# Optimization experiments

Measured on AMD Instinct MI355X. Metric: run time of the kernel, lower is better.

## Reference

```python
import jax, jax.numpy as jnp
import numpy as np
import math

B, S, D = 4, 2048, 768
H, DH = 12, 64  # num heads, head dim; H*DH == D


def setup_inputs() -> dict:
    key = jax.random.key(0)
    ks = jax.random.split(key, 10)
    q = jax.random.normal(ks[0], (B, S, D), jnp.float32)
    k = jax.random.normal(ks[1], (B, S, D), jnp.float32)
    v = jax.random.normal(ks[2], (B, S, D), jnp.float32)
    attention_mask = jax.random.bernoulli(ks[3], 0.1, (B, S, S))
    s = 1.0 / math.sqrt(D)
    # Linear weights stored as [in, out] so projection is x @ W + b
    Wq = jax.random.uniform(ks[4], (D, D), jnp.float32, -s, s)
    bq = jax.random.uniform(ks[5], (D,), jnp.float32, -s, s)
    Wk = jax.random.uniform(ks[6], (D, D), jnp.float32, -s, s)
    bk = jax.random.uniform(ks[7], (D,), jnp.float32, -s, s)
    Wv = jax.random.uniform(ks[8], (D, D), jnp.float32, -s, s)
    bv = jax.random.uniform(ks[9], (D,), jnp.float32, -s, s)
    return {"q": q, "k": k, "v": v, "attention_mask": attention_mask,
            "Wq": Wq, "bq": bq, "Wk": Wk, "bk": bk, "Wv": Wv, "bv": bv}


def _split_heads(x):
    # [B, S, D] -> [B, H, S, DH]
    return x.reshape(B, -1, H, DH).transpose(0, 2, 1, 3)


def reference(q, k, v, attention_mask, Wq, bq, Wk, bk, Wv, bv):
    Q = _split_heads(q @ Wq + bq)
    K = _split_heads(k @ Wk + bk)
    V = _split_heads(v @ Wv + bv)
    scores = jnp.einsum('bhqd,bhkd->bhqk', Q, K) / math.sqrt(DH)
    # masked_fill(mask, -1e9); 3-dim mask broadcasts over heads
    scores = jnp.where(attention_mask[:, None, :, :], -1.0e9, scores)
    probs = jax.nn.softmax(scores, axis=-1)
    ctx = jnp.einsum('bhqk,bhkd->bhqd', probs, V)
    ctx = ctx.transpose(0, 2, 1, 3).reshape(B, -1, H * DH)
    return ctx, probs
```

## Files before the change

### kernel.cpp

```cpp
#include <hip/hip_runtime.h>
#include <hip/hip_bf16.h>

#define BB 4
#define SS 2048
#define DD 768
#define HH 12
#define NE 6291456

typedef unsigned short u16t;
typedef unsigned char  u8t;
typedef unsigned int   u32t;
typedef __attribute__((ext_vector_type(8)))  short bf16x8;
typedef __attribute__((ext_vector_type(4)))  float f32x4;

union FragU { bf16x8 v; ushort4 h[2]; uint4 u; u32t g[4]; };

__device__ __forceinline__ u16t f2bf(float f) {
  union { float fv; u32t u; } x; x.fv = f;
  u32t r = x.u + 0x7FFFu + ((x.u >> 16) & 1u);
  return (u16t)(r >> 16);
}

__device__ __forceinline__ u32t pkbf2(float a, float b) {
  __hip_bfloat162 h2 = __float22bfloat162_rn(make_float2(a, b));
  union { __hip_bfloat162 h; u32t u; } c; c.h = h2;
  return c.u;
}

__device__ __forceinline__ u32t pack4(u32t w) {
  return ((w & 0x01010101u) * 0x01020408u) >> 24;
}
__device__ __forceinline__ u32t pack16b(uint4 v) {
  return pack4(v.x) | (pack4(v.y) << 4) | (pack4(v.z) << 8) | (pack4(v.w) << 12);
}
__device__ __forceinline__ u32t pack_i4(int4 v) {
  return (v.x ? 1u : 0u) | ((v.y ? 1u : 0u) << 1) | ((v.z ? 1u : 0u) << 2) | ((v.w ? 1u : 0u) << 3);
}
__device__ __forceinline__ u32t pack_f4(float4 v) {
  return (v.x != 0.f ? 1u : 0u) | ((v.y != 0.f ? 1u : 0u) << 1) |
         ((v.z != 0.f ? 1u : 0u) << 2) | ((v.w != 0.f ? 1u : 0u) << 3);
}

__global__ void detect_kernel(const u32t* __restrict__ mp, int* __restrict__ flag)
{
  __shared__ int s_isb, s_isf;
  if (threadIdx.x == 0) { s_isb = 0; s_isf = 0; }
  __syncthreads();
  int isb = 0, isf = 0;
  for (int i = threadIdx.x; i < 16384; i += 256) {
    u32t v = mp[i];
    if ((v & 0xFF000000u) == 0x3F000000u) isf = 1;
    else if (v & 0xFFFFFF00u) isb = 1;
  }
  if (isb) atomicOr(&s_isb, 1);
  if (isf) atomicOr(&s_isf, 1);
  __syncthreads();
  if (threadIdx.x == 0) *flag = s_isf ? 2 : (s_isb ? 1 : 0);
}

__global__ __launch_bounds__(256)
void mask_pack_kernel(const void* __restrict__ msk, const int* __restrict__ flagp,
                      u32t* __restrict__ pm)
{
  const int gid = blockIdx.x * 256 + threadIdx.x;
  const int row = gid >> 6, c = gid & 63;
  const int fmt = *flagp;
  const size_t src = (size_t)(row >> 11) * SS * SS + (size_t)(row & 2047) * SS + c * 32;
  u32t bits;
  if (fmt == 1) {
    const uint4* s = (const uint4*)((const u8t*)msk + src);
    bits = pack16b(s[0]) | (pack16b(s[1]) << 16);
  } else if (fmt == 0) {
    const int4* s = (const int4*)((const int*)msk + src);
    bits = 0;
#pragma unroll
    for (int j = 0; j < 8; ++j) bits |= pack_i4(s[j]) << (j * 4);
  } else {
    const float4* s = (const float4*)((const float*)msk + src);
    bits = 0;
#pragma unroll
    for (int j = 0; j < 8; ++j) bits |= pack_f4(s[j]) << (j * 4);
  }
  pm[(size_t)row * 64 + c] = bits;
}

__global__ __launch_bounds__(256)
void cvt_x_kernel(const float* __restrict__ q, const float* __restrict__ k,
                  const float* __restrict__ v, u16t* __restrict__ xb)
{
  const float* src = (blockIdx.y == 0) ? q : (blockIdx.y == 1) ? k : v;
  u16t* dst = xb + (size_t)blockIdx.y * NE;
  const size_t i = ((size_t)blockIdx.x * 256 + threadIdx.x) * 8;
  float4 f0 = *(const float4*)(src + i);
  float4 f1 = *(const float4*)(src + i + 4);
  uint4 o;
  o.x = pkbf2(f0.x, f0.y); o.y = pkbf2(f0.z, f0.w);
  o.z = pkbf2(f1.x, f1.y); o.w = pkbf2(f1.z, f1.w);
  *(uint4*)(dst + i) = o;
}

__global__ __launch_bounds__(256)
void cvt_w_kernel(const float* __restrict__ Wq, const float* __restrict__ Wk,
                  const float* __restrict__ Wv, u16t* __restrict__ Wt)
{
  __shared__ u16t T[64 * 72];
  const int t = threadIdx.x;
  const float* W = (blockIdx.z == 0) ? Wq : (blockIdx.z == 1) ? Wk : Wv;
  u16t* wt = Wt + (size_t)blockIdx.z * DD * DD;
  const int n0 = blockIdx.x * 64, k0 = blockIdx.y * 64;
  const int r = t >> 2, cs = (t & 3) * 16;
#pragma unroll
  for (int i = 0; i < 4; ++i) {
    float4 f = *(const float4*)(W + (size_t)(k0 + r) * DD + n0 + cs + i * 4);
    T[(cs + i * 4 + 0) * 72 + r] = f2bf(f.x);
    T[(cs + i * 4 + 1) * 72 + r] = f2bf(f.y);
    T[(cs + i * 4 + 2) * 72 + r] = f2bf(f.z);
    T[(cs + i * 4 + 3) * 72 + r] = f2bf(f.w);
  }
  __syncthreads();
#pragma unroll
  for (int i = 0; i < 2; ++i) {
    uint4 vv = *(const uint4*)&T[r * 72 + cs + i * 8];
    *(uint4*)(wt + (size_t)(n0 + r) * DD + k0 + cs + i * 8) = vv;
  }
}

__device__ __forceinline__ void proj_core(const u16t* __restrict__ Xrow,
    const u16t* __restrict__ Wrow, u16t* __restrict__ Ab, u16t* __restrict__ Bb,
    int t, f32x4 acc[8])
{
  const int w = t >> 6, l = t & 63;
  const int lq = l & 15, lg = l >> 4;
  const int gr = l >> 3;
  const int gc = ((l & 7) ^ (l >> 3)) * 8;

#define PSTAGE_A(kk_, buf_)                                                       \
  _Pragma("unroll")                                                               \
  for (int j = 0; j < 2; ++j) {                                                   \
    const int rr = (w * 2 + j) * 8 + gr;                                          \
    const u16t* gsrc = Xrow + (size_t)rr * DD + (kk_) + gc;                       \
    __builtin_amdgcn_global_load_lds(                                             \
        (const __attribute__((address_space(1))) void*)gsrc,                      \
        (__attribute__((address_space(3))) void*)(Ab + (buf_) * 4096 + (w * 2 + j) * 512), \
        16, 0, 0);                                                                \
  }
#define PSTAGE_B(kk_, buf_)                                                       \
  _Pragma("unroll")                                                               \
  for (int j = 0; j < 4; ++j) {                                                   \
    const int rr = (w * 4 + j) * 8 + gr;                                          \
    const u16t* gsrc = Wrow + (size_t)rr * DD + (kk_) + gc;                       \
    __builtin_amdgcn_global_load_lds(                                             \
        (const __attribute__((address_space(1))) void*)gsrc,                      \
        (__attribute__((address_space(3))) void*)(Bb + (buf_) * 8192 + (w * 4 + j) * 512), \
        16, 0, 0);                                                                \
  }

  PSTAGE_A(0, 0)
  PSTAGE_B(0, 0)
  __syncthreads();

  const int xa = (lq & 7) * 8;
  for (int kki = 0; kki < 12; ++kki) {
    const int buf = kki & 1;
    if (kki < 11) { PSTAGE_A((kki + 1) * 64, buf ^ 1) PSTAGE_B((kki + 1) * 64, buf ^ 1) }
    const int arow = w * 16 + lq;
    FragU af[2];
#pragma unroll
    for (int ks = 0; ks < 2; ++ks) {
      af[ks].h[0] = *(const ushort4*)&Ab[buf * 4096 + arow * 64 + ((ks * 32 + 4 * lg) ^ xa)];
      af[ks].h[1] = *(const ushort4*)&Ab[buf * 4096 + arow * 64 + ((ks * 32 + 4 * lg + 16) ^ xa)];
    }
#pragma unroll
    for (int nt = 0; nt < 8; ++nt) {
      const int brow = nt * 16 + lq;
#pragma unroll
      for (int ks = 0; ks < 2; ++ks) {
        FragU bf;
        bf.h[0] = *(const ushort4*)&Bb[buf * 8192 + brow * 64 + ((ks * 32 + 4 * lg) ^ xa)];
        bf.h[1] = *(const ushort4*)&Bb[buf * 8192 + brow * 64 + ((ks * 32 + 4 * lg + 16) ^ xa)];
        acc[nt] = __builtin_amdgcn_mfma_f32_16x16x32_bf16(af[ks].v, bf.v, acc[nt], 0, 0, 0);
      }
    }
    __syncthreads();
  }
#undef PSTAGE_A
#undef PSTAGE_B
}

__global__ __launch_bounds__(256, 3)
void proj_qk_kernel(const u16t* __restrict__ Xb, const u16t* __restrict__ Wt,
                    const float* __restrict__ bias, u16t* __restrict__ out)
{
  __shared__ u16t Ab[2 * 4096];
  __shared__ u16t Bb[2 * 8192];
  const int t = threadIdx.x;
  const int w = t >> 6, l = t & 63;
  const int lq = l & 15, lg = l >> 4;
  const int m0 = blockIdx.x * 64;
  const int n0 = blockIdx.y * 128;
  const int b = m0 >> 11;

  f32x4 acc[8];
#pragma unroll
  for (int i = 0; i < 8; ++i)
#pragma unroll
    for (int r = 0; r < 4; ++r) acc[i][r] = 0.f;

  proj_core(Xb + (size_t)m0 * DD, Wt + (size_t)n0 * DD, Ab, Bb, t, acc);

#pragma unroll
  for (int nt = 0; nt < 8; ++nt) {
    const int n = n0 + nt * 16 + lq;
    const int h = n >> 6, dh = n & 63;
    const float bb = bias[n];
#pragma unroll
    for (int r = 0; r < 4; ++r) {
      const int s = (m0 & 2047) + w * 16 + 4 * lg + r;
      out[((size_t)(b * HH + h) * SS + s) * 64 + dh] = f2bf(acc[nt][r] + bb);
    }
  }
}

__global__ __launch_bounds__(256, 3)
void proj_v_kernel(const u16t* __restrict__ Xb, const u16t* __restrict__ Wt,
                   const float* __restrict__ bias, u16t* __restrict__ out)
{
  __shared__ u16t Ab[2 * 4096];
  __shared__ u16t Bb[2 * 8192];
  const int t = threadIdx.x;
  const int w = t >> 6, l = t & 63;
  const int lq = l & 15, lg = l >> 4;
  const int m0 = blockIdx.x * 64;
  const int n0 = blockIdx.y * 128;
  const int b = m0 >> 11;

  f32x4 acc[8];
#pragma unroll
  for (int i = 0; i < 8; ++i)
#pragma unroll
    for (int r = 0; r < 4; ++r) acc[i][r] = 0.f;

  proj_core(Xb + (size_t)m0 * DD, Wt + (size_t)n0 * DD, Ab, Bb, t, acc);

  u16t* Tl = Bb;
#pragma unroll
  for (int nt = 0; nt < 8; ++nt) {
    const float bb = bias[n0 + nt * 16 + lq];
#pragma unroll
    for (int r = 0; r < 4; ++r)
      Tl[(nt * 16 + lq) * 72 + w * 16 + 4 * lg + r] = f2bf(acc[nt][r] + bb);
  }
  __syncthreads();

  const int rowl = t >> 1;
  const int half = t & 1;
  const int ncol = n0 + rowl;
  const int h = ncol >> 6, dh = ncol & 63;
  const int s = (m0 & 2047) + half * 32;
  u16t* dst = out + ((size_t)(b * HH + h) * 64 + dh) * SS + s;
#pragma unroll
  for (int i = 0; i < 4; ++i) {
    uint4 vv = *(const uint4*)&Tl[rowl * 72 + half * 32 + i * 8];
    *(uint4*)(dst + i * 8) = vv;
  }
}

__global__ __launch_bounds__(256, 3)
void attn_kernel(const u16t* __restrict__ Qh, const u16t* __restrict__ Kh,
                 const u16t* __restrict__ Vh, const u32t* __restrict__ pm,
                 float* __restrict__ ctx, float* __restrict__ probs)
{
  __shared__ u16t Kb3[3][64 * 64];
  __shared__ u16t Vb3[3][64 * 64];

  const int t = threadIdx.x;
  const int w = t >> 6, l = t & 63;
  const int lq = l & 15, lg = l >> 4;

  const int bid = (int)blockIdx.x;
  const int lid = (bid & 7) * 192 + (bid >> 3);
  const int bh = lid >> 5;
  const int qt = lid & 31;
  const int b = bh / HH;
  const int qbase = qt * 64 + w * 16;

  const u16t* qh = Qh + (size_t)bh * SS * 64;
  const u16t* kh = Kh + (size_t)bh * SS * 64;
  const u16t* vh = Vh + (size_t)bh * SS * 64;

  FragU bq_[2];
  {
    const u16t* qp = qh + (size_t)(qbase + lq) * 64;
#pragma unroll
    for (int ks = 0; ks < 2; ++ks) {
      bq_[ks].h[0] = *(const ushort4*)(qp + ks * 32 + 4 * lg);
      bq_[ks].h[1] = *(const ushort4*)(qp + ks * 32 + 4 * lg + 16);
    }
  }

  const u32t* mrow = pm + ((size_t)b * SS + qbase + lq) * 64;

  const float SC = 0.125f * 1.44269504f;
  const float B4 = 4.0f * 1.44269504f;

  const int gr = l >> 3;
  const int gc = ((l & 7) ^ (l >> 3)) * 8;

#define STAGE_K(kt_, buf_)                                                        \
  _Pragma("unroll")                                                               \
  for (int j = 0; j < 2; ++j) {                                                   \
    const int rr = (w * 2 + j) * 8 + gr;                                          \
    const u16t* gsrc = kh + (size_t)((kt_) * 64 + rr) * 64 + gc;                  \
    __builtin_amdgcn_global_load_lds(                                             \
        (const __attribute__((address_space(1))) void*)gsrc,                      \
        (__attribute__((address_space(3))) void*)(&Kb3[buf_][(w * 2 + j) * 512]), \
        16, 0, 0);                                                                \
  }

#define STAGE_V(kt_, buf_)                                                        \
  _Pragma("unroll")                                                               \
  for (int j = 0; j < 2; ++j) {                                                   \
    const int dv = (w * 2 + j) * 8 + gr;                                          \
    const u16t* gsrc = vh + (size_t)dv * SS + (kt_) * 64 + gc;                    \
    __builtin_amdgcn_global_load_lds(                                             \
        (const __attribute__((address_space(1))) void*)gsrc,                      \
        (__attribute__((address_space(3))) void*)(&Vb3[buf_][(w * 2 + j) * 512]), \
        16, 0, 0);                                                                \
  }

#define QKT_CHUNK(nt_, buf_, accv)                                                \
  {                                                                               \
    const int krow = (nt_) * 16 + lq;                                             \
    const int xr = (lq & 7) * 8;                                                  \
    _Pragma("unroll")                                                             \
    for (int r = 0; r < 4; ++r) (accv)[r] = 0.f;                                  \
    _Pragma("unroll")                                                             \
    for (int ks = 0; ks < 2; ++ks) {                                              \
      FragU ak;                                                                   \
      ak.h[0] = *(const ushort4*)&Kb3[buf_][krow * 64 + ((ks * 32 + 4 * lg) ^ xr)]; \
      ak.h[1] = *(const ushort4*)&Kb3[buf_][krow * 64 + ((ks * 32 + 4 * lg + 16) ^ xr)]; \
      (accv) = __builtin_amdgcn_mfma_f32_16x16x32_bf16(ak.v, bq_[ks].v, (accv), 0, 0, 0); \
    }                                                                             \
  }

  float ssum = 0.f;

  STAGE_K(0, 0)
  STAGE_K(1, 1)
  for (int kt = 0; kt < 32; ++kt) {
    if (kt == 31) { asm volatile("s_waitcnt vmcnt(0)" ::: "memory"); }
    else          { asm volatile("s_waitcnt vmcnt(2)" ::: "memory"); }
    __builtin_amdgcn_s_barrier();
    if (kt < 30) { STAGE_K(kt + 2, (kt + 2) % 3) }
    const int buf = kt % 3;
    const uint2 mw = *(const uint2*)(mrow + kt * 2);
#pragma unroll
    for (int nt = 0; nt < 4; ++nt) {
      f32x4 a;
      QKT_CHUNK(nt, buf, a)
      const u32t word = (nt < 2) ? mw.x : mw.y;
      const int sh = 16 * (nt & 1) + 4 * lg;
#pragma unroll
      for (int r = 0; r < 4; ++r) {
        float s = fmaf(a[r], SC, -B4);
        if ((word >> (sh + r)) & 1) s = -1.0e9f;
        ssum += __builtin_exp2f(s);
      }
    }
  }

  ssum += __shfl_xor(ssum, 16);
  ssum += __shfl_xor(ssum, 32);
  const float inv = 1.0f / ssum;

  f32x4 acco[4];
#pragma unroll
  for (int i = 0; i < 4; ++i)
#pragma unroll
    for (int r = 0; r < 4; ++r) acco[i][r] = 0.f;

  const size_t prow = ((size_t)bh * SS + qbase + lq) * SS;

  __builtin_amdgcn_s_barrier();
  STAGE_K(0, 0) STAGE_V(0, 0)
  STAGE_K(1, 1) STAGE_V(1, 1)

  for (int kt = 0; kt < 32; ++kt) {
    if (kt == 0)                  { asm volatile("s_waitcnt vmcnt(4)"  ::: "memory"); }
    else if (kt == 1 || kt == 31) { asm volatile("s_waitcnt vmcnt(8)"  ::: "memory"); }
    else                          { asm volatile("s_waitcnt vmcnt(12)" ::: "memory"); }
    __builtin_amdgcn_s_barrier();
    if (kt < 30) { STAGE_K(kt + 2, (kt + 2) % 3) STAGE_V(kt + 2, (kt + 2) % 3) }
    const int buf = kt % 3;
    const uint2 mw = *(const uint2*)(mrow + kt * 2);

    f32x4 sc[4];
#pragma unroll
    for (int nt = 0; nt < 4; ++nt) {
      f32x4 a;
      QKT_CHUNK(nt, buf, a)
      const u32t word = (nt < 2) ? mw.x : mw.y;
      const int sh = 16 * (nt & 1) + 4 * lg;
#pragma unroll
      for (int r = 0; r < 4; ++r) {
        float s = fmaf(a[r], SC, -B4);
        if ((word >> (sh + r)) & 1) s = -1.0e9f;
        sc[nt][r] = __builtin_exp2f(s) * inv;
      }
    }

#pragma unroll
    for (int nt = 0; nt < 4; ++nt) {
      __builtin_nontemporal_store(sc[nt], (f32x4*)(probs + prow + kt * 64 + nt * 16 + 4 * lg));
    }

    FragU pf[2];
#pragma unroll
    for (int c = 0; c < 2; ++c) {
      pf[c].g[0] = pkbf2(sc[2 * c][0],     sc[2 * c][1]);
      pf[c].g[1] = pkbf2(sc[2 * c][2],     sc[2 * c][3]);
      pf[c].g[2] = pkbf2(sc[2 * c + 1][0], sc[2 * c + 1][1]);
      pf[c].g[3] = pkbf2(sc[2 * c + 1][2], sc[2 * c + 1][3]);
    }

    __builtin_amdgcn_s_setprio(1);
#pragma unroll
    for (int c = 0; c < 2; ++c) {
#pragma unroll
      for (int n0 = 0; n0 < 4; ++n0) {
        const int dv = n0 * 16 + lq;
        const int xv = (lq & 7) * 8;
        FragU bv;
        bv.h[0] = *(const ushort4*)&Vb3[buf][dv * 64 + ((c * 32 + 4 * lg) ^ xv)];
        bv.h[1] = *(const ushort4*)&Vb3[buf][dv * 64 + ((c * 32 + 4 * lg + 16) ^ xv)];
        acco[n0] = __builtin_amdgcn_mfma_f32_16x16x32_bf16(pf[c].v, bv.v, acco[n0], 0, 0, 0);
      }
    }
    __builtin_amdgcn_s_setprio(0);
  }

  {
    const int h = bh % HH;
    const size_t cbase = (size_t)(b * SS + qbase) * DD + h * 64;
#pragma unroll
    for (int n0 = 0; n0 < 4; ++n0)
#pragma unroll
      for (int r = 0; r < 4; ++r)
        ctx[cbase + (size_t)(4 * lg + r) * DD + n0 * 16 + lq] = acco[n0][r];
  }
#undef STAGE_K
#undef STAGE_V
#undef QKT_CHUNK
}

extern "C" void kernel_launch(void* const* d_in, const int* in_sizes, int n_in,
                              void* d_out, int out_size, void* d_ws, size_t ws_size,
                              hipStream_t stream)
{
  const float* q   = (const float*)d_in[0];
  const float* k   = (const float*)d_in[1];
  const float* v   = (const float*)d_in[2];
  const void*  msk = d_in[3];
  const float* Wq  = (const float*)d_in[4];
  const float* bq  = (const float*)d_in[5];
  const float* Wk  = (const float*)d_in[6];
  const float* bk  = (const float*)d_in[7];
  const float* Wv  = (const float*)d_in[8];
  const float* bv  = (const float*)d_in[9];
  (void)in_sizes; (void)n_in; (void)out_size; (void)ws_size;

  u16t* Qb = (u16t*)d_ws;
  u16t* Kb = Qb + NE;
  u16t* Vb = Kb + NE;
  u32t* pm = (u32t*)(Vb + NE);
  int* flag = (int*)(pm + (size_t)BB * SS * 64);

  float* ctx   = (float*)d_out;
  float* probs = ctx + NE;

  u16t* Xb = (u16t*)probs;
  u16t* Wt = Xb + (size_t)3 * NE;

  detect_kernel<<<1, 256, 0, stream>>>((const u32t*)msk, flag);
  mask_pack_kernel<<<2048, 256, 0, stream>>>(msk, flag, pm);

  cvt_x_kernel<<<dim3(3072, 3), 256, 0, stream>>>(q, k, v, Xb);
  cvt_w_kernel<<<dim3(12, 12, 3), 256, 0, stream>>>(Wq, Wk, Wv, Wt);

  dim3 pg(BB * SS / 64, DD / 128);
  proj_qk_kernel<<<pg, 256, 0, stream>>>(Xb,          Wt,               bq, Qb);
  proj_qk_kernel<<<pg, 256, 0, stream>>>(Xb + NE,     Wt + DD * DD,     bk, Kb);
  proj_v_kernel <<<pg, 256, 0, stream>>>(Xb + 2 * NE, Wt + 2 * DD * DD, bv, Vb);

  attn_kernel<<<dim3(1536), 256, 0, stream>>>(Qb, Kb, Vb, pm, ctx, probs);
}
```

Measured before the change: 415.5 us.

## Merge Q/K/V projections into one launch and unroll attention loops by two

The three projection launches become a single grid with a z dimension selecting Q, K or V, so there are fewer launches and a larger wave of blocks. In the attention kernel both passes are unrolled by two with macros, and the mask words are prefetched one stage ahead alongside the K/V staging. The vmcnt wait counts are retuned to match. The extra branching on z and the hand-tuned wait counts add complexity and a risk of ordering mistakes.

```diff
diff --git a/kernel.cpp b/kernel.cpp
--- a/kernel.cpp
+++ b/kernel.cpp
@@ -188,8 +188,10 @@
 }
 
 __global__ __launch_bounds__(256, 3)
-void proj_qk_kernel(const u16t* __restrict__ Xb, const u16t* __restrict__ Wt,
-                    const float* __restrict__ bias, u16t* __restrict__ out)
+void proj_all_kernel(const u16t* __restrict__ Xb, const u16t* __restrict__ Wt,
+                     const float* __restrict__ bq, const float* __restrict__ bk,
+                     const float* __restrict__ bv,
+                     u16t* __restrict__ Qb, u16t* __restrict__ Kb, u16t* __restrict__ Vb)
 {
   __shared__ u16t Ab[2 * 4096];
   __shared__ u16t Bb[2 * 8192];
@@ -198,70 +200,54 @@
   const int lq = l & 15, lg = l >> 4;
   const int m0 = blockIdx.x * 64;
   const int n0 = blockIdx.y * 128;
+  const int z = blockIdx.z;
   const int b = m0 >> 11;
 
+  const float* bias = (z == 0) ? bq : (z == 1) ? bk : bv;
+  u16t* out = (z == 0) ? Qb : (z == 1) ? Kb : Vb;
+
   f32x4 acc[8];
 #pragma unroll
   for (int i = 0; i < 8; ++i)
 #pragma unroll
     for (int r = 0; r < 4; ++r) acc[i][r] = 0.f;
 
-  proj_core(Xb + (size_t)m0 * DD, Wt + (size_t)n0 * DD, Ab, Bb, t, acc);
-
-#pragma unroll
-  for (int nt = 0; nt < 8; ++nt) {
-    const int n = n0 + nt * 16 + lq;
-    const int h = n >> 6, dh = n & 63;
-    const float bb = bias[n];
-#pragma unroll
-    for (int r = 0; r < 4; ++r) {
-      const int s = (m0 & 2047) + w * 16 + 4 * lg + r;
-      out[((size_t)(b * HH + h) * SS + s) * 64 + dh] = f2bf(acc[nt][r] + bb);
-    }
-  }
-}
-
-__global__ __launch_bounds__(256, 3)
-void proj_v_kernel(const u16t* __restrict__ Xb, const u16t* __restrict__ Wt,
-                   const float* __restrict__ bias, u16t* __restrict__ out)
-{
-  __shared__ u16t Ab[2 * 4096];
-  __shared__ u16t Bb[2 * 8192];
-  const int t = threadIdx.x;
-  const int w = t >> 6, l = t & 63;
-  const int lq = l & 15, lg = l >> 4;
-  const int m0 = blockIdx.x * 64;
-  const int n0 = blockIdx.y * 128;
-  const int b = m0 >> 11;
-
-  f32x4 acc[8];
-#pragma unroll
-  for (int i = 0; i < 8; ++i)
-#pragma unroll
-    for (int r = 0; r < 4; ++r) acc[i][r] = 0.f;
-
-  proj_core(Xb + (size_t)m0 * DD, Wt + (size_t)n0 * DD, Ab, Bb, t, acc);
-
-  u16t* Tl = Bb;
-#pragma unroll
-  for (int nt = 0; nt < 8; ++nt) {
-    const float bb = bias[n0 + nt * 16 + lq];
-#pragma unroll
-    for (int r = 0; r < 4; ++r)
-      Tl[(nt * 16 + lq) * 72 + w * 16 + 4 * lg + r] = f2bf(acc[nt][r] + bb);
-  }
-  __syncthreads();
-
-  const int rowl = t >> 1;
-  const int half = t & 1;
-  const int ncol = n0 + rowl;
-  const int h = ncol >> 6, dh = ncol & 63;
-  const int s = (m0 & 2047) + half * 32;
-  u16t* dst = out + ((size_t)(b * HH + h) * 64 + dh) * SS + s;
-#pragma unroll
-  for (int i = 0; i < 4; ++i) {
-    uint4 vv = *(const uint4*)&Tl[rowl * 72 + half * 32 + i * 8];
-    *(uint4*)(dst + i * 8) = vv;
+  proj_core(Xb + (size_t)z * NE + (size_t)m0 * DD,
+            Wt + (size_t)z * DD * DD + (size_t)n0 * DD, Ab, Bb, t, acc);
+
+  if (z < 2) {
+#pragma unroll
+    for (int nt = 0; nt < 8; ++nt) {
+      const int n = n0 + nt * 16 + lq;
+      const int h = n >> 6, dh = n & 63;
+      const float bb = bias[n];
+#pragma unroll
+      for (int r = 0; r < 4; ++r) {
+        const int s = (m0 & 2047) + w * 16 + 4 * lg + r;
+        out[((size_t)(b * HH + h) * SS + s) * 64 + dh] = f2bf(acc[nt][r] + bb);
+      }
+    }
+  } else {
+    u16t* Tl = Bb;
+#pragma unroll
+    for (int nt = 0; nt < 8; ++nt) {
+      const float bb = bias[n0 + nt * 16 + lq];
+#pragma unroll
+      for (int r = 0; r < 4; ++r)
+        Tl[(nt * 16 + lq) * 72 + w * 16 + 4 * lg + r] = f2bf(acc[nt][r] + bb);
+    }
+    __syncthreads();
+    const int rowl = t >> 1;
+    const int half = t & 1;
+    const int ncol = n0 + rowl;
+    const int h = ncol >> 6, dh = ncol & 63;
+    const int s = (m0 & 2047) + half * 32;
+    u16t* dst = out + ((size_t)(b * HH + h) * 64 + dh) * SS + s;
+#pragma unroll
+    for (int i = 0; i < 4; ++i) {
+      uint4 vv = *(const uint4*)&Tl[rowl * 72 + half * 32 + i * 8];
+      *(uint4*)(dst + i * 8) = vv;
+    }
   }
 }
 
@@ -343,29 +329,92 @@
     }                                                                             \
   }
 
+#define COMPUTE1(buf_, mw_)                                                       \
+  {                                                                               \
+    _Pragma("unroll")                                                             \
+    for (int nt = 0; nt < 4; ++nt) {                                              \
+      f32x4 a;                                                                    \
+      QKT_CHUNK(nt, buf_, a)                                                      \
+      const u32t word = (nt < 2) ? (mw_).x : (mw_).y;                             \
+      const int sh = 16 * (nt & 1) + 4 * lg;                                      \
+      _Pragma("unroll")                                                           \
+      for (int r = 0; r < 4; ++r) {                                               \
+        float s = fmaf(a[r], SC, -B4);                                            \
+        if ((word >> (sh + r)) & 1) s = -1.0e9f;                                  \
+        ssum += __builtin_exp2f(s);                                               \
+      }                                                                           \
+    }                                                                             \
+  }
+
+#define COMPUTE2(kt_, buf_, mw_)                                                  \
+  {                                                                               \
+    f32x4 sc[4];                                                                  \
+    _Pragma("unroll")                                                             \
+    for (int nt = 0; nt < 4; ++nt) {                                              \
+      f32x4 a;                                                                    \
+      QKT_CHUNK(nt, buf_, a)                                                      \
+      const u32t word = (nt < 2) ? (mw_).x : (mw_).y;                             \
+      const int sh = 16 * (nt & 1) + 4 * lg;                                      \
+      _Pragma("unroll")                                                           \
+      for (int r = 0; r < 4; ++r) {                                               \
+        float s = fmaf(a[r], SC, -B4);                                            \
+        if ((word >> (sh + r)) & 1) s = -1.0e9f;                                  \
+        sc[nt][r] = __builtin_exp2f(s) * inv;                                     \
+      }                                                                           \
+    }                                                                             \
+    _Pragma("unroll")                                                             \
+    for (int nt = 0; nt < 4; ++nt) {                                              \
+      __builtin_nontemporal_store(sc[nt],                                         \
+          (f32x4*)(probs + prow + (kt_) * 64 + nt * 16 + 4 * lg));                \
+    }                                                                             \
+    FragU pf[2];                                                                  \
+    _Pragma("unroll")                                                             \
+    for (int c = 0; c < 2; ++c) {                                                 \
+      pf[c].g[0] = pkbf2(sc[2 * c][0],     sc[2 * c][1]);                         \
+      pf[c].g[1] = pkbf2(sc[2 * c][2],     sc[2 * c][3]);                         \
+      pf[c].g[2] = pkbf2(sc[2 * c + 1][0], sc[2 * c + 1][1]);                     \
+      pf[c].g[3] = pkbf2(sc[2 * c + 1][2], sc[2 * c + 1][3]);                     \
+    }                                                                             \
+    __builtin_amdgcn_s_setprio(1);                                                \
+    _Pragma("unroll")                                                             \
+    for (int c = 0; c < 2; ++c) {                                                 \
+      _Pragma("unroll")                                                           \
+      for (int n0 = 0; n0 < 4; ++n0) {                                            \
+        const int dv = n0 * 16 + lq;                                              \
+        const int xv = (lq & 7) * 8;                                              \
+        FragU bvv;                                                                \
+        bvv.h[0] = *(const ushort4*)&Vb3[buf_][dv * 64 + ((c * 32 + 4 * lg) ^ xv)]; \
+        bvv.h[1] = *(const ushort4*)&Vb3[buf_][dv * 64 + ((c * 32 + 4 * lg + 16) ^ xv)]; \
+        acco[n0] = __builtin_amdgcn_mfma_f32_16x16x32_bf16(pf[c].v, bvv.v, acco[n0], 0, 0, 0); \
+      }                                                                           \
+    }                                                                             \
+    __builtin_amdgcn_s_setprio(0);                                                \
+  }
+
   float ssum = 0.f;
 
   STAGE_K(0, 0)
+  uint2 mA = *(const uint2*)(mrow + 0);
   STAGE_K(1, 1)
-  for (int kt = 0; kt < 32; ++kt) {
-    if (kt == 31) { asm volatile("s_waitcnt vmcnt(0)" ::: "memory"); }
-    else          { asm volatile("s_waitcnt vmcnt(2)" ::: "memory"); }
+  uint2 mB = *(const uint2*)(mrow + 2);
+
+  for (int kt = 0; kt < 32; kt += 2) {
+    if (kt == 0) { asm volatile("s_waitcnt vmcnt(0)" ::: "memory"); }
+    else         { asm volatile("s_waitcnt vmcnt(3)" ::: "memory"); }
     __builtin_amdgcn_s_barrier();
-    if (kt < 30) { STAGE_K(kt + 2, (kt + 2) % 3) }
-    const int buf = kt % 3;
-    const uint2 mw = *(const uint2*)(mrow + kt * 2);
-#pragma unroll
-    for (int nt = 0; nt < 4; ++nt) {
-      f32x4 a;
-      QKT_CHUNK(nt, buf, a)
-      const u32t word = (nt < 2) ? mw.x : mw.y;
-      const int sh = 16 * (nt & 1) + 4 * lg;
-#pragma unroll
-      for (int r = 0; r < 4; ++r) {
-        float s = fmaf(a[r], SC, -B4);
-        if ((word >> (sh + r)) & 1) s = -1.0e9f;
-        ssum += __builtin_exp2f(s);
-      }
+    {
+      uint2 mw = mA;
+      if (kt < 30) { STAGE_K(kt + 2, (kt + 2) % 3) mA = *(const uint2*)(mrow + (kt + 2) * 2); }
+      COMPUTE1(kt % 3, mw)
+    }
+    if (kt == 0)       { asm volatile("s_waitcnt vmcnt(0)" ::: "memory"); }
+    else if (kt == 30) { asm volatile("s_waitcnt vmcnt(0)" ::: "memory"); }
+    else               { asm volatile("s_waitcnt vmcnt(3)" ::: "memory"); }
+    __builtin_amdgcn_s_barrier();
+    {
+      uint2 mw = mB;
+      if (kt < 30) { STAGE_K(kt + 3, (kt + 3) % 3) mB = *(const uint2*)(mrow + (kt + 3) * 2); }
+      COMPUTE1((kt + 1) % 3, mw)
     }
   }
 
@@ -383,60 +432,34 @@
 
   __builtin_amdgcn_s_barrier();
   STAGE_K(0, 0) STAGE_V(0, 0)
+  mA = *(const uint2*)(mrow + 0);
   STAGE_K(1, 1) STAGE_V(1, 1)
-
-  for (int kt = 0; kt < 32; ++kt) {
-    if (kt == 0)                  { asm volatile("s_waitcnt vmcnt(4)"  ::: "memory"); }
-    else if (kt == 1 || kt == 31) { asm volatile("s_waitcnt vmcnt(8)"  ::: "memory"); }
-    else                          { asm volatile("s_waitcnt vmcnt(12)" ::: "memory"); }
+  mB = *(const uint2*)(mrow + 2);
+
+  for (int kt = 0; kt < 32; kt += 2) {
+    if (kt == 0) { asm volatile("s_waitcnt vmcnt(0)" ::: "memory"); }
+    else         { asm volatile("s_waitcnt vmcnt(9)" ::: "memory"); }
     __builtin_amdgcn_s_barrier();
-    if (kt < 30) { STAGE_K(kt + 2, (kt + 2) % 3) STAGE_V(kt + 2, (kt + 2) % 3) }
-    const int buf = kt % 3;
-    const uint2 mw = *(const uint2*)(mrow + kt * 2);
-
-    f32x4 sc[4];
-#pragma unroll
-    for (int nt = 0; nt < 4; ++nt) {
-      f32x4 a;
-      QKT_CHUNK(nt, buf, a)
-      const u32t word = (nt < 2) ? mw.x : mw.y;
-      const int sh = 16 * (nt & 1) + 4 * lg;
-#pragma unroll
-      for (int r = 0; r < 4; ++r) {
-        float s = fmaf(a[r], SC, -B4);
-        if ((word >> (sh + r)) & 1) s = -1.0e9f;
-        sc[nt][r] = __builtin_exp2f(s) * inv;
+    {
+      uint2 mw = mA;
+      if (kt < 30) {
+        STAGE_K(kt + 2, (kt + 2) % 3) STAGE_V(kt + 2, (kt + 2) % 3)
+        mA = *(const uint2*)(mrow + (kt + 2) * 2);
       }
-    }
-
-#pragma unroll
-    for (int nt = 0; nt < 4; ++nt) {
-      __builtin_nontemporal_store(sc[nt], (f32x4*)(probs + prow + kt * 64 + nt * 16 + 4 * lg));
-    }
-
-    FragU pf[2];
-#pragma unroll
-    for (int c = 0; c < 2; ++c) {
-      pf[c].g[0] = pkbf2(sc[2 * c][0],     sc[2 * c][1]);
-      pf[c].g[1] = pkbf2(sc[2 * c][2],     sc[2 * c][3]);
-      pf[c].g[2] = pkbf2(sc[2 * c + 1][0], sc[2 * c + 1][1]);
-      pf[c].g[3] = pkbf2(sc[2 * c + 1][2], sc[2 * c + 1][3]);
-    }
-
-    __builtin_amdgcn_s_setprio(1);
-#pragma unroll
-    for (int c = 0; c < 2; ++c) {
-#pragma unroll
-      for (int n0 = 0; n0 < 4; ++n0) {
-        const int dv = n0 * 16 + lq;
-        const int xv = (lq & 7) * 8;
-        FragU bv;
-        bv.h[0] = *(const ushort4*)&Vb3[buf][dv * 64 + ((c * 32 + 4 * lg) ^ xv)];
-        bv.h[1] = *(const ushort4*)&Vb3[buf][dv * 64 + ((c * 32 + 4 * lg + 16) ^ xv)];
-        acco[n0] = __builtin_amdgcn_mfma_f32_16x16x32_bf16(pf[c].v, bv.v, acco[n0], 0, 0, 0);
+      COMPUTE2(kt, kt % 3, mw)
+    }
+    if (kt == 0)       { asm volatile("s_waitcnt vmcnt(0)" ::: "memory"); }
+    else if (kt == 30) { asm volatile("s_waitcnt vmcnt(4)" ::: "memory"); }
+    else               { asm volatile("s_waitcnt vmcnt(9)" ::: "memory"); }
+    __builtin_amdgcn_s_barrier();
+    {
+      uint2 mw = mB;
+      if (kt < 30) {
+        STAGE_K(kt + 3, (kt + 3) % 3) STAGE_V(kt + 3, (kt + 3) % 3)
+        mB = *(const uint2*)(mrow + (kt + 3) * 2);
       }
-    }
-    __builtin_amdgcn_s_setprio(0);
+      COMPUTE2(kt + 1, (kt + 1) % 3, mw)
+    }
   }
 
   {
@@ -451,6 +474,8 @@
 #undef STAGE_K
 #undef STAGE_V
 #undef QKT_CHUNK
+#undef COMPUTE1
+#undef COMPUTE2
 }
 
 extern "C" void kernel_launch(void* const* d_in, const int* in_sizes, int n_in,
@@ -487,10 +512,8 @@
   cvt_x_kernel<<<dim3(3072, 3), 256, 0, stream>>>(q, k, v, Xb);
   cvt_w_kernel<<<dim3(12, 12, 3), 256, 0, stream>>>(Wq, Wk, Wv, Wt);
 
-  dim3 pg(BB * SS / 64, DD / 128);
-  proj_qk_kernel<<<pg, 256, 0, stream>>>(Xb,          Wt,               bq, Qb);
-  proj_qk_kernel<<<pg, 256, 0, stream>>>(Xb + NE,     Wt + DD * DD,     bk, Kb);
-  proj_v_kernel <<<pg, 256, 0, stream>>>(Xb + 2 * NE, Wt + 2 * DD * DD, bv, Vb);
+  proj_all_kernel<<<dim3(BB * SS / 64, DD / 128, 3), 256, 0, stream>>>(
+      Xb, Wt, bq, bk, bv, Qb, Kb, Vb);
 
   attn_kernel<<<dim3(1536), 256, 0, stream>>>(Qb, Kb, Vb, pm, ctx, probs);
 }
```

New measurement: 377.3 us. -9.2%, faster.

## Merge QKV projections into one launch and stage probs through LDS for coalesced stores

Applied to the files above, without the earlier changes.

Combines the three projection launches into one grid with a z dimension selecting Q, K or V. In the attention kernel, the first softmax-sum pass now prefetches the mask words ahead, and the second pass switches from triple to double buffering of K and V. Probabilities are written to an LDS tile and read back transposed, so each row is stored with contiguous 16-byte writes instead of strided per-lane stores. This aims to cut launch overhead and make the dominant probs write fully coalesced. It adds extra LDS traffic and an lgkmcnt wait, and the shallower prefetch can expose more load latency.

```diff
diff --git a/kernel.cpp b/kernel.cpp
--- a/kernel.cpp
+++ b/kernel.cpp
@@ -188,8 +188,10 @@
 }
 
 __global__ __launch_bounds__(256, 3)
-void proj_qk_kernel(const u16t* __restrict__ Xb, const u16t* __restrict__ Wt,
-                    const float* __restrict__ bias, u16t* __restrict__ out)
+void proj_all_kernel(const u16t* __restrict__ Xb, const u16t* __restrict__ Wt,
+                     const float* __restrict__ bq, const float* __restrict__ bk,
+                     const float* __restrict__ bv,
+                     u16t* __restrict__ Qb, u16t* __restrict__ Kb, u16t* __restrict__ Vb)
 {
   __shared__ u16t Ab[2 * 4096];
   __shared__ u16t Bb[2 * 8192];
@@ -198,70 +200,54 @@
   const int lq = l & 15, lg = l >> 4;
   const int m0 = blockIdx.x * 64;
   const int n0 = blockIdx.y * 128;
+  const int z = blockIdx.z;
   const int b = m0 >> 11;
 
+  const float* bias = (z == 0) ? bq : (z == 1) ? bk : bv;
+  u16t* out = (z == 0) ? Qb : (z == 1) ? Kb : Vb;
+
   f32x4 acc[8];
 #pragma unroll
   for (int i = 0; i < 8; ++i)
 #pragma unroll
     for (int r = 0; r < 4; ++r) acc[i][r] = 0.f;
 
-  proj_core(Xb + (size_t)m0 * DD, Wt + (size_t)n0 * DD, Ab, Bb, t, acc);
-
-#pragma unroll
-  for (int nt = 0; nt < 8; ++nt) {
-    const int n = n0 + nt * 16 + lq;
-    const int h = n >> 6, dh = n & 63;
-    const float bb = bias[n];
-#pragma unroll
-    for (int r = 0; r < 4; ++r) {
-      const int s = (m0 & 2047) + w * 16 + 4 * lg + r;
-      out[((size_t)(b * HH + h) * SS + s) * 64 + dh] = f2bf(acc[nt][r] + bb);
-    }
-  }
-}
-
-__global__ __launch_bounds__(256, 3)
-void proj_v_kernel(const u16t* __restrict__ Xb, const u16t* __restrict__ Wt,
-                   const float* __restrict__ bias, u16t* __restrict__ out)
-{
-  __shared__ u16t Ab[2 * 4096];
-  __shared__ u16t Bb[2 * 8192];
-  const int t = threadIdx.x;
-  const int w = t >> 6, l = t & 63;
-  const int lq = l & 15, lg = l >> 4;
-  const int m0 = blockIdx.x * 64;
-  const int n0 = blockIdx.y * 128;
-  const int b = m0 >> 11;
-
-  f32x4 acc[8];
-#pragma unroll
-  for (int i = 0; i < 8; ++i)
-#pragma unroll
-    for (int r = 0; r < 4; ++r) acc[i][r] = 0.f;
-
-  proj_core(Xb + (size_t)m0 * DD, Wt + (size_t)n0 * DD, Ab, Bb, t, acc);
-
-  u16t* Tl = Bb;
-#pragma unroll
-  for (int nt = 0; nt < 8; ++nt) {
-    const float bb = bias[n0 + nt * 16 + lq];
-#pragma unroll
-    for (int r = 0; r < 4; ++r)
-      Tl[(nt * 16 + lq) * 72 + w * 16 + 4 * lg + r] = f2bf(acc[nt][r] + bb);
-  }
-  __syncthreads();
-
-  const int rowl = t >> 1;
-  const int half = t & 1;
-  const int ncol = n0 + rowl;
-  const int h = ncol >> 6, dh = ncol & 63;
-  const int s = (m0 & 2047) + half * 32;
-  u16t* dst = out + ((size_t)(b * HH + h) * 64 + dh) * SS + s;
-#pragma unroll
-  for (int i = 0; i < 4; ++i) {
-    uint4 vv = *(const uint4*)&Tl[rowl * 72 + half * 32 + i * 8];
-    *(uint4*)(dst + i * 8) = vv;
+  proj_core(Xb + (size_t)z * NE + (size_t)m0 * DD,
+            Wt + (size_t)z * DD * DD + (size_t)n0 * DD, Ab, Bb, t, acc);
+
+  if (z < 2) {
+#pragma unroll
+    for (int nt = 0; nt < 8; ++nt) {
+      const int n = n0 + nt * 16 + lq;
+      const int h = n >> 6, dh = n & 63;
+      const float bb = bias[n];
+#pragma unroll
+      for (int r = 0; r < 4; ++r) {
+        const int s = (m0 & 2047) + w * 16 + 4 * lg + r;
+        out[((size_t)(b * HH + h) * SS + s) * 64 + dh] = f2bf(acc[nt][r] + bb);
+      }
+    }
+  } else {
+    u16t* Tl = Bb;
+#pragma unroll
+    for (int nt = 0; nt < 8; ++nt) {
+      const float bb = bias[n0 + nt * 16 + lq];
+#pragma unroll
+      for (int r = 0; r < 4; ++r)
+        Tl[(nt * 16 + lq) * 72 + w * 16 + 4 * lg + r] = f2bf(acc[nt][r] + bb);
+    }
+    __syncthreads();
+    const int rowl = t >> 1;
+    const int half = t & 1;
+    const int ncol = n0 + rowl;
+    const int h = ncol >> 6, dh = ncol & 63;
+    const int s = (m0 & 2047) + half * 32;
+    u16t* dst = out + ((size_t)(b * HH + h) * 64 + dh) * SS + s;
+#pragma unroll
+    for (int i = 0; i < 4; ++i) {
+      uint4 vv = *(const uint4*)&Tl[rowl * 72 + half * 32 + i * 8];
+      *(uint4*)(dst + i * 8) = vv;
+    }
   }
 }
 
@@ -270,8 +256,8 @@
                  const u16t* __restrict__ Vh, const u32t* __restrict__ pm,
                  float* __restrict__ ctx, float* __restrict__ probs)
 {
-  __shared__ u16t Kb3[3][64 * 64];
-  __shared__ u16t Vb3[3][64 * 64];
+  __shared__ u16t KV[4][64 * 64];
+  __shared__ f32x4 Pl4[4][256];
 
   const int t = threadIdx.x;
   const int w = t >> 6, l = t & 63;
@@ -306,14 +292,14 @@
   const int gr = l >> 3;
   const int gc = ((l & 7) ^ (l >> 3)) * 8;
 
-#define STAGE_K(kt_, buf_)                                                        \
+#define STAGE_K(kt_, slot_)                                                       \
   _Pragma("unroll")                                                               \
   for (int j = 0; j < 2; ++j) {                                                   \
     const int rr = (w * 2 + j) * 8 + gr;                                          \
     const u16t* gsrc = kh + (size_t)((kt_) * 64 + rr) * 64 + gc;                  \
     __builtin_amdgcn_global_load_lds(                                             \
         (const __attribute__((address_space(1))) void*)gsrc,                      \
-        (__attribute__((address_space(3))) void*)(&Kb3[buf_][(w * 2 + j) * 512]), \
+        (__attribute__((address_space(3))) void*)(&KV[slot_][(w * 2 + j) * 512]), \
         16, 0, 0);                                                                \
   }
 
@@ -324,11 +310,11 @@
     const u16t* gsrc = vh + (size_t)dv * SS + (kt_) * 64 + gc;                    \
     __builtin_amdgcn_global_load_lds(                                             \
         (const __attribute__((address_space(1))) void*)gsrc,                      \
-        (__attribute__((address_space(3))) void*)(&Vb3[buf_][(w * 2 + j) * 512]), \
+        (__attribute__((address_space(3))) void*)(&KV[2 + (buf_)][(w * 2 + j) * 512]), \
         16, 0, 0);                                                                \
   }
 
-#define QKT_CHUNK(nt_, buf_, accv)                                                \
+#define QKT_CHUNK(nt_, slot_, accv)                                               \
   {                                                                               \
     const int krow = (nt_) * 16 + lq;                                             \
     const int xr = (lq & 7) * 8;                                                  \
@@ -337,23 +323,81 @@
     _Pragma("unroll")                                                             \
     for (int ks = 0; ks < 2; ++ks) {                                              \
       FragU ak;                                                                   \
-      ak.h[0] = *(const ushort4*)&Kb3[buf_][krow * 64 + ((ks * 32 + 4 * lg) ^ xr)]; \
-      ak.h[1] = *(const ushort4*)&Kb3[buf_][krow * 64 + ((ks * 32 + 4 * lg + 16) ^ xr)]; \
+      ak.h[0] = *(const ushort4*)&KV[slot_][krow * 64 + ((ks * 32 + 4 * lg) ^ xr)]; \
+      ak.h[1] = *(const ushort4*)&KV[slot_][krow * 64 + ((ks * 32 + 4 * lg + 16) ^ xr)]; \
       (accv) = __builtin_amdgcn_mfma_f32_16x16x32_bf16(ak.v, bq_[ks].v, (accv), 0, 0, 0); \
     }                                                                             \
   }
 
+#define COMPUTE1(slot_, mw_)                                                      \
+  {                                                                               \
+    _Pragma("unroll")                                                             \
+    for (int nt = 0; nt < 4; ++nt) {                                              \
+      f32x4 a;                                                                    \
+      QKT_CHUNK(nt, slot_, a)                                                     \
+      const u32t word = (nt < 2) ? (mw_).x : (mw_).y;                             \
+      const int sh = 16 * (nt & 1) + 4 * lg;                                      \
+      _Pragma("unroll")                                                           \
+      for (int r = 0; r < 4; ++r) {                                               \
+        float s = fmaf(a[r], SC, -B4);                                            \
+        if ((word >> (sh + r)) & 1) s = -1.0e9f;                                  \
+        ssum += __builtin_exp2f(s);                                               \
+      }                                                                           \
+    }                                                                             \
+  }
+
   float ssum = 0.f;
 
   STAGE_K(0, 0)
+  uint2 mA = *(const uint2*)(mrow + 0);
   STAGE_K(1, 1)
+  uint2 mB = *(const uint2*)(mrow + 2);
+
+  for (int kt = 0; kt < 32; kt += 2) {
+    if (kt == 0) { asm volatile("s_waitcnt vmcnt(0)" ::: "memory"); }
+    else         { asm volatile("s_waitcnt vmcnt(3)" ::: "memory"); }
+    __builtin_amdgcn_s_barrier();
+    {
+      uint2 mw = mA;
+      if (kt < 30) { STAGE_K(kt + 2, (kt + 2) % 3) mA = *(const uint2*)(mrow + (kt + 2) * 2); }
+      COMPUTE1(kt % 3, mw)
+    }
+    if (kt == 0 || kt == 30) { asm volatile("s_waitcnt vmcnt(0)" ::: "memory"); }
+    else                     { asm volatile("s_waitcnt vmcnt(3)" ::: "memory"); }
+    __builtin_amdgcn_s_barrier();
+    {
+      uint2 mw = mB;
+      if (kt < 30) { STAGE_K(kt + 3, (kt + 3) % 3) mB = *(const uint2*)(mrow + (kt + 3) * 2); }
+      COMPUTE1((kt + 1) % 3, mw)
+    }
+  }
+
+  ssum += __shfl_xor(ssum, 16);
+  ssum += __shfl_xor(ssum, 32);
+  const float inv = 1.0f / ssum;
+
+  f32x4 acco[4];
+#pragma unroll
+  for (int i = 0; i < 4; ++i)
+#pragma unroll
+    for (int r = 0; r < 4; ++r) acco[i][r] = 0.f;
+
+  __builtin_amdgcn_s_barrier();
+  STAGE_K(0, 0) STAGE_V(0, 0)
+  uint2 mw2 = *(const uint2*)(mrow + 0);
+
   for (int kt = 0; kt < 32; ++kt) {
-    if (kt == 31) { asm volatile("s_waitcnt vmcnt(0)" ::: "memory"); }
-    else          { asm volatile("s_waitcnt vmcnt(2)" ::: "memory"); }
+    const int buf = kt & 1;
+    if (kt == 0) { asm volatile("s_waitcnt vmcnt(1)" ::: "memory"); }
+    else         { asm volatile("s_waitcnt vmcnt(5)" ::: "memory"); }
     __builtin_amdgcn_s_barrier();
-    if (kt < 30) { STAGE_K(kt + 2, (kt + 2) % 3) }
-    const int buf = kt % 3;
-    const uint2 mw = *(const uint2*)(mrow + kt * 2);
+    uint2 mw = mw2;
+    if (kt < 31) {
+      STAGE_K(kt + 1, buf ^ 1) STAGE_V(kt + 1, buf ^ 1)
+      mw2 = *(const uint2*)(mrow + (kt + 1) * 2);
+    }
+
+    f32x4 sc[4];
 #pragma unroll
     for (int nt = 0; nt < 4; ++nt) {
       f32x4 a;
@@ -364,55 +408,13 @@
       for (int r = 0; r < 4; ++r) {
         float s = fmaf(a[r], SC, -B4);
         if ((word >> (sh + r)) & 1) s = -1.0e9f;
-        ssum += __builtin_exp2f(s);
-      }
-    }
-  }
-
-  ssum += __shfl_xor(ssum, 16);
-  ssum += __shfl_xor(ssum, 32);
-  const float inv = 1.0f / ssum;
-
-  f32x4 acco[4];
-#pragma unroll
-  for (int i = 0; i < 4; ++i)
-#pragma unroll
-    for (int r = 0; r < 4; ++r) acco[i][r] = 0.f;
-
-  const size_t prow = ((size_t)bh * SS + qbase + lq) * SS;
-
-  __builtin_amdgcn_s_barrier();
-  STAGE_K(0, 0) STAGE_V(0, 0)
-  STAGE_K(1, 1) STAGE_V(1, 1)
-
-  for (int kt = 0; kt < 32; ++kt) {
-    if (kt == 0)                  { asm volatile("s_waitcnt vmcnt(4)"  ::: "memory"); }
-    else if (kt == 1 || kt == 31) { asm volatile("s_waitcnt vmcnt(8)"  ::: "memory"); }
-    else                          { asm volatile("s_waitcnt vmcnt(12)" ::: "memory"); }
-    __builtin_amdgcn_s_barrier();
-    if (kt < 30) { STAGE_K(kt + 2, (kt + 2) % 3) STAGE_V(kt + 2, (kt + 2) % 3) }
-    const int buf = kt % 3;
-    const uint2 mw = *(const uint2*)(mrow + kt * 2);
-
-    f32x4 sc[4];
-#pragma unroll
-    for (int nt = 0; nt < 4; ++nt) {
-      f32x4 a;
-      QKT_CHUNK(nt, buf, a)
-      const u32t word = (nt < 2) ? mw.x : mw.y;
-      const int sh = 16 * (nt & 1) + 4 * lg;
-#pragma unroll
-      for (int r = 0; r < 4; ++r) {
-        float s = fmaf(a[r], SC, -B4);
-        if ((word >> (sh + r)) & 1) s = -1.0e9f;
         sc[nt][r] = __builtin_exp2f(s) * inv;
       }
     }
 
 #pragma unroll
-    for (int nt = 0; nt < 4; ++nt) {
-      __builtin_nontemporal_store(sc[nt], (f32x4*)(probs + prow + kt * 64 + nt * 16 + 4 * lg));
-    }
+    for (int nt = 0; nt < 4; ++nt)
+      Pl4[w][lq * 16 + ((nt * 4 + lg) ^ (lq & 7))] = sc[nt];
 
     FragU pf[2];
 #pragma unroll
@@ -430,13 +432,23 @@
       for (int n0 = 0; n0 < 4; ++n0) {
         const int dv = n0 * 16 + lq;
         const int xv = (lq & 7) * 8;
-        FragU bv;
-        bv.h[0] = *(const ushort4*)&Vb3[buf][dv * 64 + ((c * 32 + 4 * lg) ^ xv)];
-        bv.h[1] = *(const ushort4*)&Vb3[buf][dv * 64 + ((c * 32 + 4 * lg + 16) ^ xv)];
-        acco[n0] = __builtin_amdgcn_mfma_f32_16x16x32_bf16(pf[c].v, bv.v, acco[n0], 0, 0, 0);
+        FragU bvv;
+        bvv.h[0] = *(const ushort4*)&KV[2 + buf][dv * 64 + ((c * 32 + 4 * lg) ^ xv)];
+        bvv.h[1] = *(const ushort4*)&KV[2 + buf][dv * 64 + ((c * 32 + 4 * lg + 16) ^ xv)];
+        acco[n0] = __builtin_amdgcn_mfma_f32_16x16x32_bf16(pf[c].v, bvv.v, acco[n0], 0, 0, 0);
       }
     }
     __builtin_amdgcn_s_setprio(0);
+
+    asm volatile("s_waitcnt lgkmcnt(0)" ::: "memory");
+    __builtin_amdgcn_sched_barrier(0);
+#pragma unroll
+    for (int s4 = 0; s4 < 4; ++s4) {
+      const int row = 4 * s4 + lg;
+      const int u = l & 15;
+      f32x4 pv4 = Pl4[w][row * 16 + (u ^ (row & 7))];
+      *(f32x4*)(probs + ((size_t)bh * SS + qbase + row) * SS + kt * 64 + u * 4) = pv4;
+    }
   }
 
   {
@@ -451,6 +463,7 @@
 #undef STAGE_K
 #undef STAGE_V
 #undef QKT_CHUNK
+#undef COMPUTE1
 }
 
 extern "C" void kernel_launch(void* const* d_in, const int* in_sizes, int n_in,
@@ -487,10 +500,8 @@
   cvt_x_kernel<<<dim3(3072, 3), 256, 0, stream>>>(q, k, v, Xb);
   cvt_w_kernel<<<dim3(12, 12, 3), 256, 0, stream>>>(Wq, Wk, Wv, Wt);
 
-  dim3 pg(BB * SS / 64, DD / 128);
-  proj_qk_kernel<<<pg, 256, 0, stream>>>(Xb,          Wt,               bq, Qb);
-  proj_qk_kernel<<<pg, 256, 0, stream>>>(Xb + NE,     Wt + DD * DD,     bk, Kb);
-  proj_v_kernel <<<pg, 256, 0, stream>>>(Xb + 2 * NE, Wt + 2 * DD * DD, bv, Vb);
+  proj_all_kernel<<<dim3(BB * SS / 64, DD / 128, 3), 256, 0, stream>>>(
+      Xb, Wt, bq, bk, bv, Qb, Kb, Vb);
 
   attn_kernel<<<dim3(1536), 256, 0, stream>>>(Qb, Kb, Vb, pm, ctx, probs);
 }
```

Result: slower. 502.2 us (+20.9%).
